# Kernel tuning notes

Measured on AMD Instinct MI355X. Metric: run time of the kernel, lower is better.

## Reference

```python
import jax, jax.numpy as jnp
import numpy as np

# Longformer-style attention: blocked sliding-window (radius W) + attention to
# the first G global tokens. Source class body was truncated, so this follows
# the canonical Longformer local+global formulation.
B, S, D = 2, 4096, 1024
H, DH = 16, 64          # num_heads, head_dim (H*DH == D)
W = 256                  # one-sided window radius == block size
G = 64                   # number of global tokens (prefix)


def setup_inputs() -> dict:
    key = jax.random.key(0)
    ks = jax.random.split(key, 5)
    x = jax.random.normal(ks[0], (B, S, D), jnp.float32)
    init = 0.02
    Wq = jax.random.normal(ks[1], (D, D), jnp.float32) * init
    Wk = jax.random.normal(ks[2], (D, D), jnp.float32) * init
    Wv = jax.random.normal(ks[3], (D, D), jnp.float32) * init
    Wo = jax.random.normal(ks[4], (D, D), jnp.float32) * init
    return {"x": x, "Wq": Wq, "Wk": Wk, "Wv": Wv, "Wo": Wo}


def _split_heads(t):
    # [B,S,D] -> [B,H,S,DH]
    return t.reshape(B, S, H, DH).transpose(0, 2, 1, 3)


def _local_mask():
    nb = S // W
    blk = jnp.arange(nb)[:, None, None]
    qi = jnp.arange(W)[None, :, None]
    kj = jnp.arange(3 * W)[None, None, :]
    i_abs = blk * W + qi                    # absolute query index
    j_abs = blk * W - W + kj                # absolute key index in 3-block strip
    return ((j_abs >= 0) & (j_abs < S) &
            (jnp.abs(j_abs - i_abs) <= W) &
            (j_abs >= G))                    # global keys handled separately


def reference(x, Wq, Wk, Wv, Wo):
    nb = S // W
    scale = 1.0 / np.sqrt(DH).astype(np.float32)
    q = _split_heads(x @ Wq)                 # [B,H,S,DH]
    k = _split_heads(x @ Wk)
    v = _split_heads(x @ Wv)

    qb = q.reshape(B, H, nb, W, DH)
    pad = ((0, 0), (0, 0), (1, 1), (0, 0), (0, 0))
    kp = jnp.pad(k.reshape(B, H, nb, W, DH), pad)
    vp = jnp.pad(v.reshape(B, H, nb, W, DH), pad)
    # 3-block strips: [B,H,nb,3W,DH]
    k3 = jnp.concatenate([kp[:, :, :-2], kp[:, :, 1:-1], kp[:, :, 2:]], axis=3)
    v3 = jnp.concatenate([vp[:, :, :-2], vp[:, :, 1:-1], vp[:, :, 2:]], axis=3)

    s_loc = jnp.einsum('bhnqd,bhnkd->bhnqk', qb, k3) * scale  # [B,H,nb,W,3W]
    s_loc = jnp.where(_local_mask()[None, None], s_loc, jnp.float32(-1e9))

    kg, vg = k[:, :, :G], v[:, :, :G]        # global prefix tokens
    s_glb = jnp.einsum('bhnqd,bhgd->bhnqg', qb, kg) * scale    # [B,H,nb,W,G]

    p = jax.nn.softmax(jnp.concatenate([s_loc, s_glb], axis=-1), axis=-1)
    p_loc, p_glb = p[..., :3 * W], p[..., 3 * W:]

    out = (jnp.einsum('bhnqk,bhnkd->bhnqd', p_loc, v3) +
           jnp.einsum('bhnqg,bhgd->bhnqd', p_glb, vg))         # [B,H,nb,W,DH]
    out = out.reshape(B, H, S, DH).transpose(0, 2, 1, 3).reshape(B, S, D)
    return out @ Wo
```

## Files before the change

kernel.cpp:

```cpp
#include <hip/hip_runtime.h>

#define BB   2
#define SS   4096
#define DD   1024
#define HH   16
#define DHH  64
#define WW   256
#define GG   64
#define NBLK 16

typedef unsigned short ushort_t;
typedef short  s16x8 __attribute__((ext_vector_type(8)));
typedef float  f32x4 __attribute__((ext_vector_type(4)));

#define QSCALE 0.18033688011112042f

__device__ __forceinline__ ushort_t f2b(float f) {
  unsigned int u = __builtin_bit_cast(unsigned int, f);
  unsigned int r = (u + 0x7fffu + ((u >> 16) & 1u)) >> 16;
  return (ushort_t)r;
}

__device__ __forceinline__ ushort_t f2b1(float f) {
  unsigned int r;
  asm("v_cvt_pk_bf16_f32 %0, %1, %2" : "=v"(r) : "v"(f), "v"(f));
  return (ushort_t)r;
}

__device__ __forceinline__ float exp2f_fast(float x) {
  return __builtin_amdgcn_exp2f(x);
}

__device__ __forceinline__ void gld16(const void* g, void* l) {
  __builtin_amdgcn_global_load_lds(
      (const __attribute__((address_space(1))) void*)g,
      (__attribute__((address_space(3))) void*)l, 16, 0, 0);
}

__global__ __launch_bounds__(256) void xcast(
    const float* __restrict__ x, ushort_t* __restrict__ xb) {
  size_t i = ((size_t)blockIdx.x * 256 + threadIdx.x) * 8;
  float4 f0 = *(const float4*)&x[i];
  float4 f1 = *(const float4*)&x[i + 4];
  ushort_t t[8];
  t[0] = f2b(f0.x); t[1] = f2b(f0.y); t[2] = f2b(f0.z); t[3] = f2b(f0.w);
  t[4] = f2b(f1.x); t[5] = f2b(f1.y); t[6] = f2b(f1.z); t[7] = f2b(f1.w);
  *(uint4*)&xb[i] = *(const uint4*)t;
}

__global__ __launch_bounds__(256) void transpose_w(
    const float* __restrict__ Wq, const float* __restrict__ Wk,
    const float* __restrict__ Wv, const float* __restrict__ Wo,
    ushort_t* __restrict__ outBase) {
  const float* src = (blockIdx.z == 0) ? Wq : (blockIdx.z == 1) ? Wk
                    : (blockIdx.z == 2) ? Wv : Wo;
  ushort_t* dst = outBase + (size_t)blockIdx.z * (1024 * 1024);
  __shared__ __align__(16) ushort_t t[64][72];
  const int tid = threadIdx.x;
  const int bx = blockIdx.x * 64, by = blockIdx.y * 64;
  const int c4 = (tid & 15) * 4;
  const int r16 = tid >> 4;
  for (int rr = r16; rr < 64; rr += 16) {
    float4 f = *(const float4*)&src[(size_t)(by + rr) * 1024 + bx + c4];
    t[c4 + 0][rr] = f2b(f.x);
    t[c4 + 1][rr] = f2b(f.y);
    t[c4 + 2][rr] = f2b(f.z);
    t[c4 + 3][rr] = f2b(f.w);
  }
  __syncthreads();
  const int sr = tid >> 3;
  const int sc = (tid & 7) * 8;
  for (int rr = sr; rr < 64; rr += 32) {
    *(uint4*)&dst[(size_t)(bx + rr) * 1024 + by + sc] = *(const uint4*)&t[rr][sc];
  }
}

template <int MODE>
__global__ __launch_bounds__(512, 2) void gemm256(
    const ushort_t* __restrict__ A, const ushort_t* __restrict__ Bt,
    ushort_t* __restrict__ O0, ushort_t* __restrict__ O1,
    ushort_t* __restrict__ O2, float* __restrict__ Of, int K) {
  __shared__ __align__(16) ushort_t SH[65536];

  const int tid  = threadIdx.x;
  const int lane = tid & 63;
  const int w    = tid >> 6;
  const int quad = lane >> 4;
  const int l16  = lane & 15;
  const int wr   = w >> 2;
  const int wc   = w & 3;

  const int id  = blockIdx.x + (gridDim.x * blockIdx.y);
  const int xcd = id & 7;
  const int seq = id >> 3;
  const int nx  = (xcd << 2) + (seq & 3);
  const int ny  = seq >> 2;
  const int bm  = nx * 256;
  const int bn  = ny * 256;

  auto Aslab = [&](int buf, int kkh) -> ushort_t* {
    return &SH[(buf * 2 + kkh) * 8192];
  };
  auto Bslab = [&](int buf, int kkh) -> ushort_t* {
    return &SH[32768 + (buf * 2 + kkh) * 8192];
  };

  const int srow = tid >> 2;
  const int sch  = (tid & 3) ^ ((srow >> 1) & 3);
  const ushort_t* Ag = A + (size_t)(bm + srow) * K + sch * 8;
  const ushort_t* Bg = Bt + (size_t)(bn + srow) * K + sch * 8;

  const int chofs = ((quad ^ ((l16 >> 1) & 3)) << 3);

  auto stage = [&](ushort_t* slab, const ushort_t* g) {
    gld16(g, &slab[tid * 8]);
    gld16(g + (size_t)128 * K, &slab[4096 + tid * 8]);
  };

  f32x4 acc[8][4] = {};
  s16x8 afrag[4], bfrag[4];

  auto ldA = [&](int buf, int kkh, int i) {
    const int row = wr * 128 + i * 16 + l16;
    return *(const s16x8*)&Aslab(buf, kkh)[row * 32 + chofs];
  };
  auto ldB = [&](int buf, int kkh, int j) {
    const int row = wc * 64 + j * 16 + l16;
    return *(const s16x8*)&Bslab(buf, kkh)[row * 32 + chofs];
  };
  auto mfma16 = [&](int ih) {
    __builtin_amdgcn_s_setprio(1);
#pragma unroll
    for (int t = 0; t < 4; t++)
#pragma unroll
      for (int j = 0; j < 4; j++)
        acc[ih * 4 + t][j] = __builtin_amdgcn_mfma_f32_16x16x32_bf16(
            afrag[t], bfrag[j], acc[ih * 4 + t][j], 0, 0, 0);
    __builtin_amdgcn_s_setprio(0);
  };

  const int NT = K >> 6;

  stage(Bslab(0, 0), Bg);
  stage(Aslab(0, 0), Ag);
  stage(Bslab(0, 1), Bg + 32);
  stage(Aslab(0, 1), Ag + 32);
  asm volatile("s_waitcnt vmcnt(4)" ::: "memory");
  stage(Bslab(1, 0), Bg + 64);
  stage(Aslab(1, 0), Ag + 64);
  stage(Bslab(1, 1), Bg + 96);
  asm volatile("s_waitcnt vmcnt(6)" ::: "memory");
  __builtin_amdgcn_s_barrier();

#pragma unroll 1
  for (int kt = 0; kt < NT; ++kt) {
    const int buf = kt & 1;
#pragma unroll
    for (int j = 0; j < 4; j++) bfrag[j] = ldB(buf, 0, j);
#pragma unroll
    for (int t = 0; t < 4; t++) afrag[t] = ldA(buf, 0, t);
    if (kt + 1 < NT) stage(Aslab(buf ^ 1, 1), Ag + (size_t)(kt + 1) * 64 + 32);
    __builtin_amdgcn_s_barrier();
    asm volatile("s_waitcnt lgkmcnt(0)" ::: "memory");
    mfma16(0);
    __builtin_amdgcn_s_barrier();
#pragma unroll
    for (int t = 0; t < 4; t++) afrag[t] = ldA(buf, 0, 4 + t);
    if (kt + 2 < NT) stage(Bslab(buf, 0), Bg + (size_t)(kt + 2) * 64);
    __builtin_amdgcn_s_barrier();
    asm volatile("s_waitcnt lgkmcnt(0)" ::: "memory");
    mfma16(1);
    __builtin_amdgcn_s_barrier();
#pragma unroll
    for (int j = 0; j < 4; j++) bfrag[j] = ldB(buf, 1, j);
#pragma unroll
    for (int t = 0; t < 4; t++) afrag[t] = ldA(buf, 1, t);
    if (kt + 2 < NT) stage(Aslab(buf, 0), Ag + (size_t)(kt + 2) * 64);
    __builtin_amdgcn_s_barrier();
    asm volatile("s_waitcnt lgkmcnt(0)" ::: "memory");
    mfma16(0);
    __builtin_amdgcn_s_barrier();
#pragma unroll
    for (int t = 0; t < 4; t++) afrag[t] = ldA(buf, 1, 4 + t);
    if (kt + 2 < NT) {
      stage(Bslab(buf, 1), Bg + (size_t)(kt + 2) * 64 + 32);
      asm volatile("s_waitcnt vmcnt(6)" ::: "memory");
    } else if (kt + 1 < NT) {
      asm volatile("s_waitcnt vmcnt(0)" ::: "memory");
    }
    __builtin_amdgcn_s_barrier();
    asm volatile("s_waitcnt lgkmcnt(0)" ::: "memory");
    mfma16(1);
    __builtin_amdgcn_s_barrier();
  }

  if (MODE == 0 && bn >= 2048) {
    const int bb = bm >> 12;
    const int n1b = bn & 1023;
    const int sb  = bm & 4095;
#pragma unroll 1
    for (int p = 0; p < 2; p++) {
      __syncthreads();
      if (wr == p) {
#pragma unroll
        for (int i = 0; i < 8; i++)
#pragma unroll
          for (int j = 0; j < 4; j++)
#pragma unroll
            for (int r = 0; r < 4; r++)
              SH[(wc * 64 + j * 16 + l16) * 136 + i * 16 + quad * 4 + r] =
                  f2b(acc[i][j][r]);
      }
      __syncthreads();
#pragma unroll
      for (int it = 0; it < 8; it++) {
        const int row = it * 32 + (tid >> 4);
        const int n1 = n1b + row;
        const int dh = n1 & 63, hh = n1 >> 6;
        const int s = sb + p * 128 + (tid & 15) * 8;
        uint4 val = *(const uint4*)&SH[row * 136 + (tid & 15) * 8];
        *(uint4*)&O2[(((size_t)bb * HH + hh) * DHH + dh) * SS + s] = val;
      }
    }
  } else {
#pragma unroll
    for (int i = 0; i < 8; i++) {
#pragma unroll
      for (int j = 0; j < 4; j++) {
#pragma unroll
        for (int r = 0; r < 4; r++) {
          int m = bm + wr * 128 + i * 16 + quad * 4 + r;
          int n = bn + wc * 64 + j * 16 + l16;
          float av = acc[i][j][r];
          if (MODE == 0) {
            int n1 = n & 1023;
            int h = n1 >> 6, dh = n1 & 63;
            int b = m >> 12, s = m & 4095;
            if (n < 1024) {
              O0[(((size_t)b * HH + h) * SS + s) * DHH + dh] = f2b(av * QSCALE);
            } else {
              O1[(((size_t)b * HH + h) * SS + s) * DHH + dh] = f2b(av);
            }
          } else {
            Of[(size_t)m * DD + n] = av;
          }
        }
      }
    }
  }
}

__global__ __launch_bounds__(256, 2) void attn_kernel(
    const ushort_t* __restrict__ q, const ushort_t* __restrict__ k,
    const ushort_t* __restrict__ vT, ushort_t* __restrict__ out) {
  const int blk = blockIdx.x;
  const int h   = blockIdx.y;
  const int b   = blockIdx.z;
  const int tid  = threadIdx.x;
  const int lane = tid & 63;
  const int w    = tid >> 6;
  const int quad = lane >> 4;
  const int l16  = lane & 15;

  const size_t bh = ((size_t)b * HH + h) * SS * DHH;
  const ushort_t* qb  = q + bh;
  const ushort_t* kb  = k + bh;
  const ushort_t* vtb = vT + bh;

  __shared__ __align__(16) ushort_t Ps[4][64 * 64];
  ushort_t* Pw = &Ps[w][0];

  const int q0 = blk * WW + w * 64;

  const int wbase = ((l16 >> 3) << 9) + (quad << 5) + (l16 & 7);
  const int rbase = (quad << 9) + (l16 << 3);

  s16x8 aq[4][2];
#pragma unroll
  for (int mt = 0; mt < 4; mt++)
#pragma unroll
    for (int x = 0; x < 2; x++)
      aq[mt][x] = *(const s16x8*)&qb[(size_t)(q0 + mt * 16 + l16) * DHH + x * 32 + quad * 8];

  f32x4 oacc[4][4] = {};
  f32x4 rsacc[4] = {};

  s16x8 vone;
#pragma unroll
  for (int j = 0; j < 8; j++) vone[j] = (short)0x3F80;

  s16x8 bk[4][2];
  s16x8 bv[4][2];

  auto LOADK = [&](int j0s) {
    const ushort_t* kc = kb + (size_t)j0s * DHH;
#pragma unroll
    for (int nt = 0; nt < 4; nt++)
#pragma unroll
      for (int x = 0; x < 2; x++)
        bk[nt][x] = *(const s16x8*)&kc[(nt * 16 + l16) * DHH + x * 32 + quad * 8];
  };
  auto LOADV = [&](int j0s) {
    const ushort_t* vc = vtb + j0s;
#pragma unroll
    for (int dt = 0; dt < 4; dt++)
#pragma unroll
      for (int x = 0; x < 2; x++)
        bv[dt][x] = *(const s16x8*)&vc[(size_t)(dt * 16 + l16) * SS + x * 32 + quad * 8];
  };

  const int jlo = (q0 - (int)WW < (int)GG) ? (int)GG : (q0 - (int)WW);
  int jhi = q0 + (int)WW;
  if (jhi > SS - 64) jhi = SS - 64;

  int j0  = jlo;
  int j0u = __builtin_amdgcn_readfirstlane(j0);
  LOADK(j0u);

  bool last = false;
  while (!last) {
    int jn = j0 + 64;
    if (j0 == 0) { last = true; jn = 0; }
    else if (jn > jhi) jn = 0;

    LOADV(j0u);

    const int dlt = j0 - q0;
    const bool needmask = (j0 != 0) && (dlt < -193 || dlt > 193);

#pragma unroll
    for (int nt = 0; nt < 4; nt++) {
      const int j = j0 + nt * 16 + l16;
#pragma unroll
      for (int mt = 0; mt < 4; mt++) {
        f32x4 s4 = {0.f, 0.f, 0.f, 0.f};
        s4 = __builtin_amdgcn_mfma_f32_16x16x32_bf16(aq[mt][0], bk[nt][0], s4, 0, 0, 0);
        s4 = __builtin_amdgcn_mfma_f32_16x16x32_bf16(aq[mt][1], bk[nt][1], s4, 0, 0, 0);
#pragma unroll
        for (int r = 0; r < 4; r++) {
          float p;
          if (needmask) {
            int i = q0 + mt * 16 + quad * 4 + r;
            int d = j - i;
            p = (d <= (int)WW && d >= -(int)WW) ? exp2f_fast(s4[r]) : 0.0f;
          } else {
            p = exp2f_fast(s4[r]);
          }
          Pw[wbase + nt * 1024 + mt * 128 + r * 8] = f2b1(p);
        }
      }
    }

    int jnu = __builtin_amdgcn_readfirstlane(jn);
    if (!last) LOADK(jnu);

    __builtin_amdgcn_s_setprio(1);
#pragma unroll
    for (int ll = 0; ll < 64; ll += 32) {
      s16x8 ap[4];
#pragma unroll
      for (int mt = 0; mt < 4; mt++)
        ap[mt] = *(const s16x8*)&Pw[rbase + (ll >> 3) * 512 + mt * 128];
#pragma unroll
      for (int mt = 0; mt < 4; mt++) {
        rsacc[mt] = __builtin_amdgcn_mfma_f32_16x16x32_bf16(ap[mt], vone, rsacc[mt], 0, 0, 0);
#pragma unroll
        for (int dt = 0; dt < 4; dt++)
          oacc[mt][dt] = __builtin_amdgcn_mfma_f32_16x16x32_bf16(ap[mt], bv[dt][ll >> 5], oacc[mt][dt], 0, 0, 0);
      }
    }
    __builtin_amdgcn_s_setprio(0);

    j0 = jn; j0u = jnu;
  }

#pragma unroll
  for (int mt = 0; mt < 4; mt++) {
#pragma unroll
    for (int r = 0; r < 4; r++) {
      float inv = __builtin_amdgcn_rcpf(rsacc[mt][r]);
      int srow2 = q0 + mt * 16 + quad * 4 + r;
      size_t orow = ((size_t)b * SS + srow2) * DD + h * DHH;
#pragma unroll
      for (int dt = 0; dt < 4; dt++)
        out[orow + dt * 16 + l16] = f2b1(oacc[mt][dt][r] * inv);
    }
  }
}

extern "C" void kernel_launch(void* const* d_in, const int* in_sizes, int n_in,
                              void* d_out, int out_size, void* d_ws, size_t ws_size,
                              hipStream_t stream) {
  const float *x, *Wq, *Wk, *Wv, *Wo;
  if (n_in == 5 && in_sizes[4] == 8388608) {
    Wk = (const float*)d_in[0]; Wo = (const float*)d_in[1];
    Wq = (const float*)d_in[2]; Wv = (const float*)d_in[3];
    x  = (const float*)d_in[4];
  } else {
    x  = (const float*)d_in[0]; Wq = (const float*)d_in[1];
    Wk = (const float*)d_in[2]; Wv = (const float*)d_in[3];
    Wo = (const float*)d_in[4];
  }
  float* out = (float*)d_out;

  char* ws = (char*)d_ws;
  ushort_t* wqkvT = (ushort_t*)(ws);
  ushort_t* woT   = (ushort_t*)(ws + 6291456);
  ushort_t* qbuf  = (ushort_t*)(ws + 8388608);
  ushort_t* kbuf  = (ushort_t*)(ws + 8388608 + 16777216);
  ushort_t* vbuf  = (ushort_t*)(ws + 8388608 + 2 * 16777216);
  ushort_t* attn  = (ushort_t*)(ws + 8388608 + 3 * 16777216);
  ushort_t* xb    = attn;

  xcast<<<dim3(4096), 256, 0, stream>>>(x, xb);
  transpose_w<<<dim3(16, 16, 4), 256, 0, stream>>>(Wq, Wk, Wv, Wo, wqkvT);
  gemm256<0><<<dim3(32, 12), 512, 0, stream>>>(xb, wqkvT, qbuf, kbuf, vbuf, nullptr, 1024);
  attn_kernel<<<dim3(NBLK, HH, BB), 256, 0, stream>>>(qbuf, kbuf, vbuf, attn);
  gemm256<1><<<dim3(32, 4), 512, 0, stream>>>(attn, woT, nullptr, nullptr, nullptr, out, 1024);
}
```

Measured before the change: 245.9 us.

## Use a dedicated 128x128-tile GEMM for the output projection

Result: faster. 239.1 us (-2.8%).

```diff
diff --git a/kernel.cpp b/kernel.cpp
--- a/kernel.cpp
+++ b/kernel.cpp
@@ -14,6 +14,8 @@
 typedef float  f32x4 __attribute__((ext_vector_type(4)));
 
 #define QSCALE 0.18033688011112042f
+
+#define VMCNT(n) asm volatile("s_waitcnt vmcnt(" #n ")" ::: "memory")
 
 __device__ __forceinline__ ushort_t f2b(float f) {
   unsigned int u = __builtin_bit_cast(unsigned int, f);
@@ -75,7 +77,6 @@
   }
 }
 
-template <int MODE>
 __global__ __launch_bounds__(512, 2) void gemm256(
     const ushort_t* __restrict__ A, const ushort_t* __restrict__ Bt,
     ushort_t* __restrict__ O0, ushort_t* __restrict__ O1,
@@ -145,11 +146,11 @@
   stage(Aslab(0, 0), Ag);
   stage(Bslab(0, 1), Bg + 32);
   stage(Aslab(0, 1), Ag + 32);
-  asm volatile("s_waitcnt vmcnt(4)" ::: "memory");
+  VMCNT(4);
   stage(Bslab(1, 0), Bg + 64);
   stage(Aslab(1, 0), Ag + 64);
   stage(Bslab(1, 1), Bg + 96);
-  asm volatile("s_waitcnt vmcnt(6)" ::: "memory");
+  VMCNT(6);
   __builtin_amdgcn_s_barrier();
 
 #pragma unroll 1
@@ -184,9 +185,9 @@
     for (int t = 0; t < 4; t++) afrag[t] = ldA(buf, 1, 4 + t);
     if (kt + 2 < NT) {
       stage(Bslab(buf, 1), Bg + (size_t)(kt + 2) * 64 + 32);
-      asm volatile("s_waitcnt vmcnt(6)" ::: "memory");
+      VMCNT(6);
     } else if (kt + 1 < NT) {
-      asm volatile("s_waitcnt vmcnt(0)" ::: "memory");
+      VMCNT(0);
     }
     __builtin_amdgcn_s_barrier();
     asm volatile("s_waitcnt lgkmcnt(0)" ::: "memory");
@@ -194,7 +195,7 @@
     __builtin_amdgcn_s_barrier();
   }
 
-  if (MODE == 0 && bn >= 2048) {
+  if (bn >= 2048) {
     const int bb = bm >> 12;
     const int n1b = bn & 1023;
     const int sb  = bm & 4095;
@@ -232,19 +233,105 @@
           int m = bm + wr * 128 + i * 16 + quad * 4 + r;
           int n = bn + wc * 64 + j * 16 + l16;
           float av = acc[i][j][r];
-          if (MODE == 0) {
-            int n1 = n & 1023;
-            int h = n1 >> 6, dh = n1 & 63;
-            int b = m >> 12, s = m & 4095;
-            if (n < 1024) {
-              O0[(((size_t)b * HH + h) * SS + s) * DHH + dh] = f2b(av * QSCALE);
-            } else {
-              O1[(((size_t)b * HH + h) * SS + s) * DHH + dh] = f2b(av);
-            }
+          int n1 = n & 1023;
+          int h = n1 >> 6, dh = n1 & 63;
+          int b = m >> 12, s = m & 4095;
+          if (n < 1024) {
+            O0[(((size_t)b * HH + h) * SS + s) * DHH + dh] = f2b(av * QSCALE);
           } else {
-            Of[(size_t)m * DD + n] = av;
+            O1[(((size_t)b * HH + h) * SS + s) * DHH + dh] = f2b(av);
           }
         }
+      }
+    }
+  }
+}
+
+__global__ __launch_bounds__(256, 4) void gemmk128(
+    const ushort_t* __restrict__ A, const ushort_t* __restrict__ Bt,
+    float* __restrict__ Of, int K) {
+  __shared__ __align__(16) ushort_t As[2][128 * 32];
+  __shared__ __align__(16) ushort_t Bs[2][128 * 32];
+
+  const int tid  = threadIdx.x;
+  const int lane = tid & 63;
+  const int w    = tid >> 6;
+  const int quad = lane >> 4;
+  const int l16  = lane & 15;
+  const int wr   = w >> 1;
+  const int wc   = w & 1;
+
+  const int id  = blockIdx.x + (gridDim.x * blockIdx.y);
+  const int xcd = id & 7;
+  const int seq = id >> 3;
+  const int nx  = (xcd << 3) + (seq & 7);
+  const int ny  = seq >> 3;
+  const int bm  = nx * 128;
+  const int bn  = ny * 128;
+
+  const int srow = tid >> 2;
+  const int sch  = (tid & 3) ^ ((srow >> 1) & 3);
+  const ushort_t* Ag = A + (size_t)(bm + srow) * K + sch * 8;
+  const ushort_t* Bg = Bt + (size_t)(bn + srow) * K + sch * 8;
+  const int sch2 = (tid & 3) ^ (((srow + 64) >> 1) & 3);
+  const ushort_t* Ag2 = A + (size_t)(bm + srow + 64) * K + sch2 * 8;
+  const ushort_t* Bg2 = Bt + (size_t)(bn + srow + 64) * K + sch2 * 8;
+
+  const int chofs = ((quad ^ ((l16 >> 1) & 3)) << 3);
+
+  auto stage = [&](int buf, int s) {
+    gld16(Ag + (size_t)s * 32, &As[buf][tid * 8]);
+    gld16(Ag2 + (size_t)s * 32, &As[buf][2048 + tid * 8]);
+    gld16(Bg + (size_t)s * 32, &Bs[buf][tid * 8]);
+    gld16(Bg2 + (size_t)s * 32, &Bs[buf][2048 + tid * 8]);
+  };
+
+  f32x4 acc[4][4] = {};
+
+  const int NT = K >> 5;
+
+  stage(0, 0);
+  VMCNT(0);
+  __builtin_amdgcn_s_barrier();
+
+#pragma unroll 1
+  for (int s = 0; s < NT; ++s) {
+    const int buf = s & 1;
+    if (s + 1 < NT) {
+      stage(buf ^ 1, s + 1);
+      VMCNT(4);
+    } else {
+      VMCNT(0);
+    }
+    __builtin_amdgcn_s_barrier();
+    s16x8 afrag[4], bfrag[4];
+#pragma unroll
+    for (int t = 0; t < 4; t++)
+      afrag[t] = *(const s16x8*)&As[buf][(wr * 64 + t * 16 + l16) * 32 + chofs];
+#pragma unroll
+    for (int j = 0; j < 4; j++)
+      bfrag[j] = *(const s16x8*)&Bs[buf][(wc * 64 + j * 16 + l16) * 32 + chofs];
+    asm volatile("s_waitcnt lgkmcnt(0)" ::: "memory");
+    __builtin_amdgcn_s_setprio(1);
+#pragma unroll
+    for (int t = 0; t < 4; t++)
+#pragma unroll
+      for (int j = 0; j < 4; j++)
+        acc[t][j] = __builtin_amdgcn_mfma_f32_16x16x32_bf16(
+            afrag[t], bfrag[j], acc[t][j], 0, 0, 0);
+    __builtin_amdgcn_s_setprio(0);
+    __builtin_amdgcn_s_barrier();
+  }
+
+#pragma unroll
+  for (int i = 0; i < 4; i++) {
+#pragma unroll
+    for (int j = 0; j < 4; j++) {
+#pragma unroll
+      for (int r = 0; r < 4; r++) {
+        int m = bm + wr * 64 + i * 16 + quad * 4 + r;
+        int n = bn + wc * 64 + j * 16 + l16;
+        Of[(size_t)m * DD + n] = acc[i][j][r];
       }
     }
   }
@@ -414,7 +501,7 @@
 
   xcast<<<dim3(4096), 256, 0, stream>>>(x, xb);
   transpose_w<<<dim3(16, 16, 4), 256, 0, stream>>>(Wq, Wk, Wv, Wo, wqkvT);
-  gemm256<0><<<dim3(32, 12), 512, 0, stream>>>(xb, wqkvT, qbuf, kbuf, vbuf, nullptr, 1024);
+  gemm256<<<dim3(32, 12), 512, 0, stream>>>(xb, wqkvT, qbuf, kbuf, vbuf, nullptr, 1024);
   attn_kernel<<<dim3(NBLK, HH, BB), 256, 0, stream>>>(qbuf, kbuf, vbuf, attn);
-  gemm256<1><<<dim3(32, 4), 512, 0, stream>>>(attn, woT, nullptr, nullptr, nullptr, out, 1024);
-}
+  gemmk128<<<dim3(64, 8), 256, 0, stream>>>(attn, woT, out, 1024);
+}
```
